# Kernel tuning notes

Measured on AMD Instinct MI355X. Metric: run time of the kernel, lower is better.

## Reference

```python
import jax, jax.numpy as jnp
import numpy as np

DIM = 768
NUM_HEAD = 12
DIM_HEAD = DIM // NUM_HEAD
SCALE = DIM_HEAD ** -0.5
B, N = 4, 1024


def setup_inputs() -> dict:
    key = jax.random.key(0)
    ks = jax.random.split(key, 6)
    return {
        "x": jax.random.normal(ks[0], (B, N, DIM), jnp.float32),
        "q_weight": jax.random.normal(ks[1], (DIM, DIM), jnp.float32) * 0.02,
        "k_weight": jax.random.normal(ks[2], (DIM, DIM), jnp.float32) * 0.02,
        "v_weight": jax.random.normal(ks[3], (DIM, DIM), jnp.float32) * 0.02,
        "q_bias": jnp.zeros((DIM,), jnp.float32),
        "k_bias": jnp.zeros((DIM,), jnp.float32),
        "v_bias": jnp.zeros((DIM,), jnp.float32),
        "proj_weight": jax.random.normal(ks[4], (DIM, DIM), jnp.float32) * 0.02,
        "proj_bias": jax.random.normal(ks[5], (DIM,), jnp.float32) * 0.02,
    }


def reference(x, q_weight, k_weight, v_weight, q_bias, k_bias, v_bias,
              proj_weight, proj_bias):
    B_, N_, C = x.shape
    shortcut = x
    # pre-norm: torch .std() is unbiased (ddof=1)
    mean = jnp.mean(x, axis=-1, keepdims=True)
    std = jnp.std(x, axis=-1, keepdims=True, ddof=1)
    xn = (x - mean) / std
    # F.linear: x @ W.T + b
    q = xn @ q_weight.T + q_bias
    k = xn @ k_weight.T + k_bias
    v = xn @ v_weight.T + v_bias
    # b n (h d) -> b h n d
    q = q.reshape(B_, N_, NUM_HEAD, DIM_HEAD).transpose(0, 2, 1, 3)
    k = k.reshape(B_, N_, NUM_HEAD, DIM_HEAD).transpose(0, 2, 1, 3)
    v = v.reshape(B_, N_, NUM_HEAD, DIM_HEAD).transpose(0, 2, 1, 3)
    attn = jnp.einsum('bhqd,bhkd->bhqk', q, k * SCALE)
    attn = jax.nn.softmax(attn, axis=-1)
    out = jnp.einsum('bhqk,bhkd->bhqd', attn, v)
    out = out.transpose(0, 2, 1, 3).reshape(B_, N_, C)
    out = out @ proj_weight.T + proj_bias
    return out + shortcut
```

## Files before the change

### kernel.cpp

```cpp
#include <hip/hip_runtime.h>

typedef unsigned short ushort_t;
typedef unsigned int uint_t;
typedef __attribute__((ext_vector_type(8))) unsigned short ushort8;
typedef __attribute__((ext_vector_type(2))) unsigned int uint2v;
typedef __attribute__((ext_vector_type(8))) __bf16 bf16x8;
typedef __attribute__((ext_vector_type(4))) float floatx4;

#define DIM 768
#define NHEAD 12
#define DHEAD 64
#define SEQ 1024
#define BATCH 4
#define TOKENS (BATCH * SEQ)
#define WELEM (DIM * DIM)
#define SCALE_LOG2E 0.18033688011112042f

static __device__ __forceinline__ uint_t fbits(float f) {
  union { float f; uint_t u; } c; c.f = f; return c.u;
}
static __device__ __forceinline__ ushort_t f2bf(float f) {
  return (ushort_t)((fbits(f) + 0x8000u) >> 16);
}
static __device__ __forceinline__ uint_t pack_bf2(float lo, float hi) {
  const uint_t a = fbits(lo) + 0x8000u, b = fbits(hi) + 0x8000u;
#if __has_builtin(__builtin_amdgcn_perm)
  return __builtin_amdgcn_perm(b, a, 0x07060302u);
#else
  return (a >> 16) | (b & 0xFFFF0000u);
#endif
}
static __device__ __forceinline__ floatx4 mfma16(ushort8 a, ushort8 b, floatx4 c) {
  return __builtin_amdgcn_mfma_f32_16x16x32_bf16(
      __builtin_bit_cast(bf16x8, a), __builtin_bit_cast(bf16x8, b), c, 0, 0, 0);
}
static __device__ __forceinline__ void gload_lds16(const ushort_t* g,
                                                   ushort_t* l) {
  __builtin_amdgcn_global_load_lds(
      (const __attribute__((address_space(1))) void*)g,
      (__attribute__((address_space(3))) void*)l, 16, 0, 0);
}

__global__ __launch_bounds__(256) void cvt_kernel(
    const float* __restrict__ qw, const float* __restrict__ kw,
    const float* __restrict__ vw, const float* __restrict__ pw,
    ushort_t* __restrict__ dst) {
  const float* s = (blockIdx.y == 0) ? qw : (blockIdx.y == 1) ? kw
                  : (blockIdx.y == 2) ? vw : pw;
  ushort_t* d = dst + (size_t)blockIdx.y * WELEM;
  const int i = (blockIdx.x * 256 + threadIdx.x) * 4;
  const float4 f = *(const float4*)&s[i];
  uint2v o;
  o[0] = pack_bf2(f.x, f.y);
  o[1] = pack_bf2(f.z, f.w);
  *(uint2v*)&d[i] = o;
}

__global__ __launch_bounds__(256) void ln_kernel(const float* __restrict__ x,
                                                 ushort_t* __restrict__ xn) {
  const int wave = threadIdx.x >> 6, lane = threadIdx.x & 63;
  const int row = blockIdx.x * 4 + wave;
  const float4* xr = (const float4*)(x + (size_t)row * DIM);
  float4 v[3];
  float s = 0.f, s2 = 0.f;
#pragma unroll
  for (int j = 0; j < 3; ++j) {
    v[j] = xr[j * 64 + lane];
    s += v[j].x + v[j].y + v[j].z + v[j].w;
    s2 += v[j].x * v[j].x + v[j].y * v[j].y + v[j].z * v[j].z + v[j].w * v[j].w;
  }
#pragma unroll
  for (int off = 1; off < 64; off <<= 1) {
    s += __shfl_xor(s, off);
    s2 += __shfl_xor(s2, off);
  }
  const float mean = s * (1.f / 768.f);
  const float var = (s2 - 768.f * mean * mean) * (1.f / 767.f);
  const float rstd = rsqrtf(var);
  ushort_t* xo = xn + (size_t)row * DIM;
#pragma unroll
  for (int j = 0; j < 3; ++j) {
    uint2v o;
    o[0] = pack_bf2((v[j].x - mean) * rstd, (v[j].y - mean) * rstd);
    o[1] = pack_bf2((v[j].z - mean) * rstd, (v[j].w - mean) * rstd);
    *(uint2v*)&xo[(j * 64 + lane) * 4] = o;
  }
}

#define BK 64
__global__ __launch_bounds__(256) void qkv_kernel(
    const ushort_t* __restrict__ xn, const ushort_t* __restrict__ wbf,
    const float* __restrict__ qb, const float* __restrict__ kb,
    const float* __restrict__ vb,
    ushort_t* __restrict__ qh, ushort_t* __restrict__ kh,
    ushort_t* __restrict__ vt) {
  __shared__ ushort_t As[128 * BK];
  __shared__ ushort_t Bs[128 * BK];
  const int tid = threadIdx.x;
  const int wave = tid >> 6, lane = tid & 63, quad = lane >> 4, l15 = lane & 15;
  const int m0 = blockIdx.x * 128;
  const int mat = blockIdx.y / 6, nb = blockIdx.y % 6;
  const int n0 = nb * 128;
  const ushort_t* W = wbf + (size_t)mat * WELEM;
  const int wm = (wave >> 1) * 64, wn = (wave & 1) * 64;
  const int srow8 = lane >> 3;
  const int schunk = (lane & 7) ^ srow8;
  const int l7 = l15 & 7;

  floatx4 acc[4][4];
#pragma unroll
  for (int i = 0; i < 4; ++i)
#pragma unroll
    for (int j = 0; j < 4; ++j) acc[i][j] = (floatx4){0.f, 0.f, 0.f, 0.f};

  for (int k0 = 0; k0 < DIM; k0 += BK) {
#pragma unroll
    for (int i = 0; i < 4; ++i) {
      const int c = wave * 4 + i;
      const int row = c * 8 + srow8;
      gload_lds16(&xn[(size_t)(m0 + row) * DIM + k0 + schunk * 8], &As[c * 512]);
      gload_lds16(&W[(size_t)(n0 + row) * DIM + k0 + schunk * 8], &Bs[c * 512]);
    }
    __syncthreads();
    ushort8 af[4][2], bfr[4][2];
#pragma unroll
    for (int i = 0; i < 4; ++i)
#pragma unroll
      for (int k2 = 0; k2 < 2; ++k2) {
        const int ch = ((k2 * 4 + quad) ^ l7) * 8;
        af[i][k2] = *(const ushort8*)&As[(wm + i * 16 + l15) * BK + ch];
        bfr[i][k2] = *(const ushort8*)&Bs[(wn + i * 16 + l15) * BK + ch];
      }
    if (mat != 2) {
#pragma unroll
      for (int k2 = 0; k2 < 2; ++k2)
#pragma unroll
        for (int i = 0; i < 4; ++i)
#pragma unroll
          for (int j = 0; j < 4; ++j)
            acc[i][j] = mfma16(af[i][k2], bfr[j][k2], acc[i][j]);
    } else {
#pragma unroll
      for (int k2 = 0; k2 < 2; ++k2)
#pragma unroll
        for (int i = 0; i < 4; ++i)
#pragma unroll
          for (int j = 0; j < 4; ++j)
            acc[i][j] = mfma16(bfr[i][k2], af[j][k2], acc[i][j]);
    }
    __syncthreads();
  }

  if (mat != 2) {
    const float* bias = (mat == 0) ? qb : kb;
    ushort_t* dst = (mat == 0) ? qh : kh;
    const float oscale = (mat == 0) ? SCALE_LOG2E : 1.0f;
#pragma unroll
    for (int i = 0; i < 4; ++i) {
#pragma unroll
      for (int j = 0; j < 4; ++j) {
        const int col = n0 + wn + j * 16 + l15;
        const float bv = bias[col];
        const int hh = col >> 6, d = col & 63;
#pragma unroll
        for (int r = 0; r < 4; ++r) {
          const int rowg = m0 + wm + i * 16 + quad * 4 + r;
          const int bb = rowg >> 10, nn = rowg & 1023;
          dst[(size_t)(((bb * NHEAD + hh) * SEQ) + nn) * DHEAD + d] =
              f2bf((acc[i][j][r] + bv) * oscale);
        }
      }
    }
  } else {
#pragma unroll
    for (int i = 0; i < 4; ++i) {
#pragma unroll
      for (int j = 0; j < 4; ++j) {
        const int tokb = m0 + wm + j * 16;
        const int tok = tokb + l15;
        const int bb = tok >> 10, nn = tok & 1023;
        const int t2 = (nn >> 4) & 3;
        const int goff = (nn & ~63) + l15 * 4 + t2;
#pragma unroll
        for (int r = 0; r < 4; ++r) {
          const int ch = n0 + wn + i * 16 + quad * 4 + r;
          const int hh = ch >> 6, d = ch & 63;
          vt[(size_t)(((bb * NHEAD + hh) * DHEAD) + d) * SEQ + goff] =
              f2bf(acc[i][j][r] + vb[ch]);
        }
      }
    }
  }
}

#define PSTR 68
__global__ __launch_bounds__(128) void attn_kernel(
    const ushort_t* __restrict__ qh, const ushort_t* __restrict__ kh,
    const ushort_t* __restrict__ vt, ushort_t* __restrict__ ao) {
  __shared__ ushort_t Ks[64 * 64];
  __shared__ ushort_t Vts[64 * 64];
  __shared__ ushort_t Ps[2][2][16 * PSTR];
  const int tid = threadIdx.x;
  const int wave = tid >> 6, lane = tid & 63, quad = lane >> 4, l15 = lane & 15;
  const int l7 = l15 & 7;
  const int h = blockIdx.y, b = blockIdx.z;
  const int basekv = ((b * NHEAD + h) * SEQ) * DHEAD;
  const int basevt = ((b * NHEAD + h) * DHEAD) * SEQ;
  const int q0 = blockIdx.x * 64 + wave * 32;

  ushort8 qf[2][2];
#pragma unroll
  for (int w = 0; w < 2; ++w) {
    const ushort_t* Qr = qh + basekv + (q0 + w * 16 + l15) * DHEAD;
    qf[w][0] = *(const ushort8*)&Qr[quad * 8];
    qf[w][1] = *(const ushort8*)&Qr[32 + quad * 8];
  }
  ushort8 ones;
#pragma unroll
  for (int i = 0; i < 8; ++i) ones[i] = 0x3F80;

  floatx4 o[2][4];
#pragma unroll
  for (int w = 0; w < 2; ++w)
#pragma unroll
    for (int t = 0; t < 4; ++t) o[w][t] = (floatx4){0.f, 0.f, 0.f, 0.f};
  floatx4 acc_l[2] = {(floatx4){0.f, 0.f, 0.f, 0.f},
                      (floatx4){0.f, 0.f, 0.f, 0.f}};

  const int srow8 = lane >> 3, schunk = (lane & 7) ^ srow8;

  for (int kt = 0; kt < SEQ; kt += 64) {
#pragma unroll
    for (int i = 0; i < 4; ++i) {
      const int c = wave * 4 + i;
      gload_lds16(&kh[basekv + (kt + c * 8 + srow8) * DHEAD + schunk * 8],
                  &Ks[c * 512]);
      gload_lds16(&vt[basevt + (c * 8 + srow8) * SEQ + kt + schunk * 8],
                  &Vts[c * 512]);
    }
    __syncthreads();

    floatx4 sacc[2][4];
#pragma unroll
    for (int w = 0; w < 2; ++w)
#pragma unroll
      for (int s = 0; s < 4; ++s) sacc[w][s] = (floatx4){0.f, 0.f, 0.f, 0.f};
#pragma unroll
    for (int s = 0; s < 4; ++s) {
#pragma unroll
      for (int hh = 0; hh < 2; ++hh) {
        const ushort8 kf = *(const ushort8*)&Ks[(s * 16 + l15) * 64 +
                                                (((hh * 4 + quad) ^ l7) * 8)];
#pragma unroll
        for (int w = 0; w < 2; ++w)
          sacc[w][s] = mfma16(qf[w][hh], kf, sacc[w][s]);
      }
    }

#pragma unroll
    for (int w = 0; w < 2; ++w) {
#pragma unroll
      for (int r = 0; r < 4; ++r) {
        uint2v pk;
        pk[0] = pack_bf2(exp2f(sacc[w][0][r]), exp2f(sacc[w][1][r]));
        pk[1] = pack_bf2(exp2f(sacc[w][2][r]), exp2f(sacc[w][3][r]));
        *(uint2v*)&Ps[wave][w][(quad * 4 + r) * PSTR + l15 * 4] = pk;
      }
    }

#pragma unroll
    for (int hh = 0; hh < 2; ++hh) {
      ushort8 pf[2];
#pragma unroll
      for (int w = 0; w < 2; ++w) {
        pf[w] = *(const ushort8*)&Ps[wave][w][l15 * PSTR + hh * 32 + quad * 8];
        acc_l[w] = mfma16(pf[w], ones, acc_l[w]);
      }
#pragma unroll
      for (int t = 0; t < 4; ++t) {
        const ushort8 vf = *(const ushort8*)&Vts[(t * 16 + l15) * 64 +
                                                 (((hh * 4 + quad) ^ l7) * 8)];
#pragma unroll
        for (int w = 0; w < 2; ++w) o[w][t] = mfma16(pf[w], vf, o[w][t]);
      }
    }
    __syncthreads();
  }

#pragma unroll
  for (int w = 0; w < 2; ++w) {
#pragma unroll
    for (int r = 0; r < 4; ++r) {
      const float rl = 1.f / acc_l[w][r];
      const int token = b * SEQ + q0 + w * 16 + quad * 4 + r;
#pragma unroll
      for (int t = 0; t < 4; ++t)
        ao[(size_t)token * DIM + h * DHEAD + t * 16 + l15] =
            f2bf(o[w][t][r] * rl);
    }
  }
}

__global__ __launch_bounds__(256) void proj_kernel(
    const ushort_t* __restrict__ ao, const ushort_t* __restrict__ pwb,
    const float* __restrict__ pb, const float* __restrict__ x,
    float* __restrict__ out) {
  __shared__ ushort_t As[64 * BK];
  __shared__ ushort_t Bs[128 * BK];
  const int tid = threadIdx.x;
  const int wave = tid >> 6, lane = tid & 63, quad = lane >> 4, l15 = lane & 15;
  const int m0 = blockIdx.x * 64;
  const int n0 = blockIdx.y * 128;
  const int wm = (wave >> 1) * 32, wn = (wave & 1) * 64;
  const int srow8 = lane >> 3;
  const int schunk = (lane & 7) ^ srow8;
  const int l7 = l15 & 7;

  floatx4 acc[2][4];
#pragma unroll
  for (int i = 0; i < 2; ++i)
#pragma unroll
    for (int j = 0; j < 4; ++j) acc[i][j] = (floatx4){0.f, 0.f, 0.f, 0.f};

  for (int k0 = 0; k0 < DIM; k0 += BK) {
#pragma unroll
    for (int i = 0; i < 2; ++i) {
      const int c = wave * 2 + i;
      const int row = c * 8 + srow8;
      gload_lds16(&ao[(size_t)(m0 + row) * DIM + k0 + schunk * 8], &As[c * 512]);
    }
#pragma unroll
    for (int i = 0; i < 4; ++i) {
      const int c = wave * 4 + i;
      const int row = c * 8 + srow8;
      gload_lds16(&pwb[(size_t)(n0 + row) * DIM + k0 + schunk * 8], &Bs[c * 512]);
    }
    __syncthreads();
    ushort8 af[2][2], bfr[4][2];
#pragma unroll
    for (int k2 = 0; k2 < 2; ++k2) {
      const int ch = ((k2 * 4 + quad) ^ l7) * 8;
#pragma unroll
      for (int i = 0; i < 2; ++i)
        af[i][k2] = *(const ushort8*)&As[(wm + i * 16 + l15) * BK + ch];
#pragma unroll
      for (int j = 0; j < 4; ++j)
        bfr[j][k2] = *(const ushort8*)&Bs[(wn + j * 16 + l15) * BK + ch];
    }
#pragma unroll
    for (int k2 = 0; k2 < 2; ++k2)
#pragma unroll
      for (int i = 0; i < 2; ++i)
#pragma unroll
        for (int j = 0; j < 4; ++j)
          acc[i][j] = mfma16(af[i][k2], bfr[j][k2], acc[i][j]);
    __syncthreads();
  }

#pragma unroll
  for (int i = 0; i < 2; ++i) {
#pragma unroll
    for (int j = 0; j < 4; ++j) {
      const int col = n0 + wn + j * 16 + l15;
      const float bv = pb[col];
#pragma unroll
      for (int r = 0; r < 4; ++r) {
        const int rowg = m0 + wm + i * 16 + quad * 4 + r;
        out[(size_t)rowg * DIM + col] =
            acc[i][j][r] + bv + x[(size_t)rowg * DIM + col];
      }
    }
  }
}

extern "C" void kernel_launch(void* const* d_in, const int* in_sizes, int n_in,
                              void* d_out, int out_size, void* d_ws,
                              size_t ws_size, hipStream_t stream) {
  const float* x  = (const float*)d_in[0];
  const float* qw = (const float*)d_in[1];
  const float* kw = (const float*)d_in[2];
  const float* vw = (const float*)d_in[3];
  const float* qb = (const float*)d_in[4];
  const float* kb = (const float*)d_in[5];
  const float* vb = (const float*)d_in[6];
  const float* pw = (const float*)d_in[7];
  const float* pb = (const float*)d_in[8];
  float* out = (float*)d_out;

  ushort_t* ws = (ushort_t*)d_ws;
  const size_t NTOK = (size_t)TOKENS * DIM;
  ushort_t* xn  = ws;
  ushort_t* qh  = ws + NTOK;
  ushort_t* kh  = ws + 2 * NTOK;
  ushort_t* vt  = ws + 3 * NTOK;
  ushort_t* wbf = ws + 4 * NTOK;
  ushort_t* ao  = xn;

  cvt_kernel<<<dim3(WELEM / 1024, 4), 256, 0, stream>>>(qw, kw, vw, pw, wbf);
  ln_kernel<<<TOKENS / 4, 256, 0, stream>>>(x, xn);
  qkv_kernel<<<dim3(32, 18), 256, 0, stream>>>(xn, wbf, qb, kb, vb, qh, kh, vt);
  attn_kernel<<<dim3(16, NHEAD, BATCH), 128, 0, stream>>>(qh, kh, vt, ao);
  proj_kernel<<<dim3(64, 6), 256, 0, stream>>>(ao, wbf + 3 * (size_t)WELEM, pb,
                                               x, out);
}
```

Baseline: 171.0 us.

## Split attention KV range across wave groups; transpose GEMM outputs for vector stores

The attention kernel now runs 256 threads per block. Two wave groups each process half of the key/value sequence for the same queries, and the partial outputs and row sums are merged through shared memory. The QKV and projection GEMMs swap operand roles so each lane holds four consecutive channels, which allows packed bf16 and float4 stores and vectorised bias and residual loads. A hardware exp2 builtin replaces exp2f. The split adds a shared-memory reduction and an extra barrier at the end of attention, and it depends on the softmax having no running max (scores are exponentiated directly).

```diff
diff --git a/kernel.cpp b/kernel.cpp
--- a/kernel.cpp
+++ b/kernel.cpp
@@ -28,6 +28,13 @@
   return __builtin_amdgcn_perm(b, a, 0x07060302u);
 #else
   return (a >> 16) | (b & 0xFFFF0000u);
+#endif
+}
+static __device__ __forceinline__ float fexp2(float x) {
+#if __has_builtin(__builtin_amdgcn_exp2f)
+  return __builtin_amdgcn_exp2f(x);
+#else
+  return exp2f(x);
 #endif
 }
 static __device__ __forceinline__ floatx4 mfma16(ushort8 a, ushort8 b, floatx4 c) {
@@ -102,7 +109,7 @@
   const int mat = blockIdx.y / 6, nb = blockIdx.y % 6;
   const int n0 = nb * 128;
   const ushort_t* W = wbf + (size_t)mat * WELEM;
-  const int wm = (wave >> 1) * 64, wn = (wave & 1) * 64;
+  const int chan_off = (wave >> 1) * 64, tok_off = (wave & 1) * 64;
   const int srow8 = lane >> 3;
   const int schunk = (lane & 7) ^ srow8;
   const int l7 = l15 & 7;
@@ -128,85 +135,77 @@
 #pragma unroll
       for (int k2 = 0; k2 < 2; ++k2) {
         const int ch = ((k2 * 4 + quad) ^ l7) * 8;
-        af[i][k2] = *(const ushort8*)&As[(wm + i * 16 + l15) * BK + ch];
-        bfr[i][k2] = *(const ushort8*)&Bs[(wn + i * 16 + l15) * BK + ch];
-      }
-    if (mat != 2) {
-#pragma unroll
-      for (int k2 = 0; k2 < 2; ++k2)
-#pragma unroll
-        for (int i = 0; i < 4; ++i)
-#pragma unroll
-          for (int j = 0; j < 4; ++j)
-            acc[i][j] = mfma16(af[i][k2], bfr[j][k2], acc[i][j]);
-    } else {
-#pragma unroll
-      for (int k2 = 0; k2 < 2; ++k2)
-#pragma unroll
-        for (int i = 0; i < 4; ++i)
-#pragma unroll
-          for (int j = 0; j < 4; ++j)
-            acc[i][j] = mfma16(bfr[i][k2], af[j][k2], acc[i][j]);
-    }
+        bfr[i][k2] = *(const ushort8*)&Bs[(chan_off + i * 16 + l15) * BK + ch];
+        af[i][k2] = *(const ushort8*)&As[(tok_off + i * 16 + l15) * BK + ch];
+      }
+#pragma unroll
+    for (int k2 = 0; k2 < 2; ++k2)
+#pragma unroll
+      for (int i = 0; i < 4; ++i)
+#pragma unroll
+        for (int j = 0; j < 4; ++j)
+          acc[i][j] = mfma16(bfr[i][k2], af[j][k2], acc[i][j]);
     __syncthreads();
   }
 
   if (mat != 2) {
     const float* bias = (mat == 0) ? qb : kb;
     ushort_t* dst = (mat == 0) ? qh : kh;
-    const float oscale = (mat == 0) ? SCALE_LOG2E : 1.0f;
+    const float os = (mat == 0) ? SCALE_LOG2E : 1.0f;
+    const int hh = (n0 + chan_off) >> 6;
 #pragma unroll
     for (int i = 0; i < 4; ++i) {
+      const int ch0 = n0 + chan_off + i * 16 + quad * 4;
+      const float4 bv = *(const float4*)&bias[ch0];
+      const int d0 = i * 16 + quad * 4;
 #pragma unroll
       for (int j = 0; j < 4; ++j) {
-        const int col = n0 + wn + j * 16 + l15;
-        const float bv = bias[col];
-        const int hh = col >> 6, d = col & 63;
-#pragma unroll
-        for (int r = 0; r < 4; ++r) {
-          const int rowg = m0 + wm + i * 16 + quad * 4 + r;
-          const int bb = rowg >> 10, nn = rowg & 1023;
-          dst[(size_t)(((bb * NHEAD + hh) * SEQ) + nn) * DHEAD + d] =
-              f2bf((acc[i][j][r] + bv) * oscale);
-        }
+        const int tok = m0 + tok_off + j * 16 + l15;
+        const int bb = tok >> 10, nn = tok & 1023;
+        uint2v pk;
+        pk[0] = pack_bf2((acc[i][j][0] + bv.x) * os, (acc[i][j][1] + bv.y) * os);
+        pk[1] = pack_bf2((acc[i][j][2] + bv.z) * os, (acc[i][j][3] + bv.w) * os);
+        *(uint2v*)&dst[(size_t)((bb * NHEAD + hh) * SEQ + nn) * DHEAD + d0] = pk;
       }
     }
   } else {
 #pragma unroll
     for (int i = 0; i < 4; ++i) {
+      const int ch0 = n0 + chan_off + i * 16 + quad * 4;
+      const float4 bv = *(const float4*)&vb[ch0];
+      const float bvf[4] = {bv.x, bv.y, bv.z, bv.w};
+      const int hh = ch0 >> 6, d0 = ch0 & 63;
 #pragma unroll
       for (int j = 0; j < 4; ++j) {
-        const int tokb = m0 + wm + j * 16;
-        const int tok = tokb + l15;
+        const int tok = m0 + tok_off + j * 16 + l15;
         const int bb = tok >> 10, nn = tok & 1023;
         const int t2 = (nn >> 4) & 3;
         const int goff = (nn & ~63) + l15 * 4 + t2;
-#pragma unroll
-        for (int r = 0; r < 4; ++r) {
-          const int ch = n0 + wn + i * 16 + quad * 4 + r;
-          const int hh = ch >> 6, d = ch & 63;
-          vt[(size_t)(((bb * NHEAD + hh) * DHEAD) + d) * SEQ + goff] =
-              f2bf(acc[i][j][r] + vb[ch]);
-        }
+        const size_t base = (size_t)((bb * NHEAD + hh) * DHEAD + d0) * SEQ;
+#pragma unroll
+        for (int r = 0; r < 4; ++r)
+          vt[base + (size_t)r * SEQ + goff] = f2bf(acc[i][j][r] + bvf[r]);
       }
     }
   }
 }
 
 #define PSTR 68
-__global__ __launch_bounds__(128) void attn_kernel(
+__global__ __launch_bounds__(256) void attn_kernel(
     const ushort_t* __restrict__ qh, const ushort_t* __restrict__ kh,
     const ushort_t* __restrict__ vt, ushort_t* __restrict__ ao) {
-  __shared__ ushort_t Ks[64 * 64];
-  __shared__ ushort_t Vts[64 * 64];
-  __shared__ ushort_t Ps[2][2][16 * PSTR];
+  __shared__ ushort_t kv[2][2][4096];
+  __shared__ ushort_t Ps[4][16 * PSTR];
+  float* cb = (float*)&kv[0][0][0];
   const int tid = threadIdx.x;
   const int wave = tid >> 6, lane = tid & 63, quad = lane >> 4, l15 = lane & 15;
   const int l7 = l15 & 7;
+  const int grp = wave >> 1, wsub = wave & 1;
   const int h = blockIdx.y, b = blockIdx.z;
   const int basekv = ((b * NHEAD + h) * SEQ) * DHEAD;
   const int basevt = ((b * NHEAD + h) * DHEAD) * SEQ;
-  const int q0 = blockIdx.x * 64 + wave * 32;
+  const int q0 = blockIdx.x * 64 + wsub * 32;
+  const int kbase = grp * 512;
 
   ushort8 qf[2][2];
 #pragma unroll
@@ -229,14 +228,14 @@
 
   const int srow8 = lane >> 3, schunk = (lane & 7) ^ srow8;
 
-  for (int kt = 0; kt < SEQ; kt += 64) {
+  for (int kt = 0; kt < 512; kt += 64) {
 #pragma unroll
     for (int i = 0; i < 4; ++i) {
-      const int c = wave * 4 + i;
-      gload_lds16(&kh[basekv + (kt + c * 8 + srow8) * DHEAD + schunk * 8],
-                  &Ks[c * 512]);
-      gload_lds16(&vt[basevt + (c * 8 + srow8) * SEQ + kt + schunk * 8],
-                  &Vts[c * 512]);
+      const int c = wsub * 4 + i;
+      gload_lds16(&kh[basekv + (kbase + kt + c * 8 + srow8) * DHEAD + schunk * 8],
+                  &kv[grp][0][c * 512]);
+      gload_lds16(&vt[basevt + (c * 8 + srow8) * SEQ + kbase + kt + schunk * 8],
+                  &kv[grp][1][c * 512]);
     }
     __syncthreads();
 
@@ -249,8 +248,8 @@
     for (int s = 0; s < 4; ++s) {
 #pragma unroll
       for (int hh = 0; hh < 2; ++hh) {
-        const ushort8 kf = *(const ushort8*)&Ks[(s * 16 + l15) * 64 +
-                                                (((hh * 4 + quad) ^ l7) * 8)];
+        const ushort8 kf = *(const ushort8*)&kv[grp][0][(s * 16 + l15) * 64 +
+                                                        (((hh * 4 + quad) ^ l7) * 8)];
 #pragma unroll
         for (int w = 0; w < 2; ++w)
           sacc[w][s] = mfma16(qf[w][hh], kf, sacc[w][s]);
@@ -262,9 +261,9 @@
 #pragma unroll
       for (int r = 0; r < 4; ++r) {
         uint2v pk;
-        pk[0] = pack_bf2(exp2f(sacc[w][0][r]), exp2f(sacc[w][1][r]));
-        pk[1] = pack_bf2(exp2f(sacc[w][2][r]), exp2f(sacc[w][3][r]));
-        *(uint2v*)&Ps[wave][w][(quad * 4 + r) * PSTR + l15 * 4] = pk;
+        pk[0] = pack_bf2(fexp2(sacc[w][0][r]), fexp2(sacc[w][1][r]));
+        pk[1] = pack_bf2(fexp2(sacc[w][2][r]), fexp2(sacc[w][3][r]));
+        *(uint2v*)&Ps[wave][(quad * 4 + r) * PSTR + l15 * 4] = pk;
       }
     }
 
@@ -273,13 +272,13 @@
       ushort8 pf[2];
 #pragma unroll
       for (int w = 0; w < 2; ++w) {
-        pf[w] = *(const ushort8*)&Ps[wave][w][l15 * PSTR + hh * 32 + quad * 8];
+        pf[w] = *(const ushort8*)&Ps[wave][l15 * PSTR + hh * 32 + quad * 8];
         acc_l[w] = mfma16(pf[w], ones, acc_l[w]);
       }
 #pragma unroll
       for (int t = 0; t < 4; ++t) {
-        const ushort8 vf = *(const ushort8*)&Vts[(t * 16 + l15) * 64 +
-                                                 (((hh * 4 + quad) ^ l7) * 8)];
+        const ushort8 vf = *(const ushort8*)&kv[grp][1][(t * 16 + l15) * 64 +
+                                                        (((hh * 4 + quad) ^ l7) * 8)];
 #pragma unroll
         for (int w = 0; w < 2; ++w) o[w][t] = mfma16(pf[w], vf, o[w][t]);
       }
@@ -287,16 +286,37 @@
     __syncthreads();
   }
 
-#pragma unroll
-  for (int w = 0; w < 2; ++w) {
-#pragma unroll
-    for (int r = 0; r < 4; ++r) {
-      const float rl = 1.f / acc_l[w][r];
-      const int token = b * SEQ + q0 + w * 16 + quad * 4 + r;
+  const int cb0 = wsub * (32 * 66);
+  if (grp == 1) {
+#pragma unroll
+    for (int w = 0; w < 2; ++w) {
 #pragma unroll
       for (int t = 0; t < 4; ++t)
-        ao[(size_t)token * DIM + h * DHEAD + t * 16 + l15] =
-            f2bf(o[w][t][r] * rl);
+#pragma unroll
+        for (int r = 0; r < 4; ++r)
+          cb[cb0 + (w * 16 + quad * 4 + r) * 66 + t * 16 + l15] = o[w][t][r];
+      if (l15 == 0)
+#pragma unroll
+        for (int r = 0; r < 4; ++r)
+          cb[cb0 + (w * 16 + quad * 4 + r) * 66 + 64] = acc_l[w][r];
+    }
+  }
+  __syncthreads();
+  if (grp == 0) {
+#pragma unroll
+    for (int w = 0; w < 2; ++w) {
+#pragma unroll
+      for (int r = 0; r < 4; ++r) {
+        const int row = w * 16 + quad * 4 + r;
+        const float l = acc_l[w][r] + cb[cb0 + row * 66 + 64];
+        const float rl = 1.f / l;
+        const int token = b * SEQ + q0 + row;
+#pragma unroll
+        for (int t = 0; t < 4; ++t) {
+          const float val = o[w][t][r] + cb[cb0 + row * 66 + t * 16 + l15];
+          ao[(size_t)token * DIM + h * DHEAD + t * 16 + l15] = f2bf(val * rl);
+        }
+      }
     }
   }
 }
@@ -311,16 +331,16 @@
   const int wave = tid >> 6, lane = tid & 63, quad = lane >> 4, l15 = lane & 15;
   const int m0 = blockIdx.x * 64;
   const int n0 = blockIdx.y * 128;
-  const int wm = (wave >> 1) * 32, wn = (wave & 1) * 64;
+  const int chan_off = (wave >> 1) * 64, tok_off = (wave & 1) * 32;
   const int srow8 = lane >> 3;
   const int schunk = (lane & 7) ^ srow8;
   const int l7 = l15 & 7;
 
-  floatx4 acc[2][4];
-#pragma unroll
-  for (int i = 0; i < 2; ++i)
-#pragma unroll
-    for (int j = 0; j < 4; ++j) acc[i][j] = (floatx4){0.f, 0.f, 0.f, 0.f};
+  floatx4 acc[4][2];
+#pragma unroll
+  for (int i = 0; i < 4; ++i)
+#pragma unroll
+    for (int j = 0; j < 2; ++j) acc[i][j] = (floatx4){0.f, 0.f, 0.f, 0.f};
 
   for (int k0 = 0; k0 < DIM; k0 += BK) {
 #pragma unroll
@@ -341,34 +361,36 @@
     for (int k2 = 0; k2 < 2; ++k2) {
       const int ch = ((k2 * 4 + quad) ^ l7) * 8;
 #pragma unroll
-      for (int i = 0; i < 2; ++i)
-        af[i][k2] = *(const ushort8*)&As[(wm + i * 16 + l15) * BK + ch];
-#pragma unroll
-      for (int j = 0; j < 4; ++j)
-        bfr[j][k2] = *(const ushort8*)&Bs[(wn + j * 16 + l15) * BK + ch];
+      for (int j = 0; j < 2; ++j)
+        af[j][k2] = *(const ushort8*)&As[(tok_off + j * 16 + l15) * BK + ch];
+#pragma unroll
+      for (int i = 0; i < 4; ++i)
+        bfr[i][k2] = *(const ushort8*)&Bs[(chan_off + i * 16 + l15) * BK + ch];
     }
 #pragma unroll
     for (int k2 = 0; k2 < 2; ++k2)
 #pragma unroll
-      for (int i = 0; i < 2; ++i)
-#pragma unroll
-        for (int j = 0; j < 4; ++j)
-          acc[i][j] = mfma16(af[i][k2], bfr[j][k2], acc[i][j]);
-    __syncthreads();
-  }
-
-#pragma unroll
-  for (int i = 0; i < 2; ++i) {
-#pragma unroll
-    for (int j = 0; j < 4; ++j) {
-      const int col = n0 + wn + j * 16 + l15;
-      const float bv = pb[col];
-#pragma unroll
-      for (int r = 0; r < 4; ++r) {
-        const int rowg = m0 + wm + i * 16 + quad * 4 + r;
-        out[(size_t)rowg * DIM + col] =
-            acc[i][j][r] + bv + x[(size_t)rowg * DIM + col];
-      }
+      for (int i = 0; i < 4; ++i)
+#pragma unroll
+        for (int j = 0; j < 2; ++j)
+          acc[i][j] = mfma16(bfr[i][k2], af[j][k2], acc[i][j]);
+    __syncthreads();
+  }
+
+#pragma unroll
+  for (int i = 0; i < 4; ++i) {
+    const int ch0 = n0 + chan_off + i * 16 + quad * 4;
+    const float4 bv = *(const float4*)&pb[ch0];
+#pragma unroll
+    for (int j = 0; j < 2; ++j) {
+      const int tok = m0 + tok_off + j * 16 + l15;
+      const float4 res = *(const float4*)&x[(size_t)tok * DIM + ch0];
+      float4 ov;
+      ov.x = acc[i][j][0] + bv.x + res.x;
+      ov.y = acc[i][j][1] + bv.y + res.y;
+      ov.z = acc[i][j][2] + bv.z + res.z;
+      ov.w = acc[i][j][3] + bv.w + res.w;
+      *(float4*)&out[(size_t)tok * DIM + ch0] = ov;
     }
   }
 }
@@ -399,7 +421,7 @@
   cvt_kernel<<<dim3(WELEM / 1024, 4), 256, 0, stream>>>(qw, kw, vw, pw, wbf);
   ln_kernel<<<TOKENS / 4, 256, 0, stream>>>(x, xn);
   qkv_kernel<<<dim3(32, 18), 256, 0, stream>>>(xn, wbf, qb, kb, vb, qh, kh, vt);
-  attn_kernel<<<dim3(16, NHEAD, BATCH), 128, 0, stream>>>(qh, kh, vt, ao);
+  attn_kernel<<<dim3(16, NHEAD, BATCH), 256, 0, stream>>>(qh, kh, vt, ao);
   proj_kernel<<<dim3(64, 6), 256, 0, stream>>>(ao, wbf + 3 * (size_t)WELEM, pb,
                                                x, out);
 }
```

Measured after the change: 159.4 us. -6.8%, faster.
